# Performance work log

Measured on AMD Instinct MI355X. Metric: run time of the kernel, lower is better.

The kernel has to match this reference:

```python
import jax, jax.numpy as jnp
import numpy as np

EPS = 1e-8
VOX_WIDTH = 1.0
CURV_THRESH = 0.5


def _build_kernels():
    """Nine 3x3x3 central finite-difference stencils, pre-divided by vox_width / vox_width^2."""
    def zk():
        return np.zeros((3, 3, 3), np.float32)
    ks = {}
    # first derivatives (central difference), denominator vox_width
    for name, ax in (('ddx', 0), ('ddy', 1), ('ddz', 2)):
        k = zk(); i = [1, 1, 1]
        i[ax] = 0; k[tuple(i)] = -0.5
        i[ax] = 2; k[tuple(i)] = 0.5
        ks[name] = k / VOX_WIDTH
    # pure second derivatives, denominator vox_width^2
    for name, ax in (('d2dx2', 0), ('d2dy2', 1), ('d2dz2', 2)):
        k = zk(); i = [1, 1, 1]
        i[ax] = 0; k[tuple(i)] = 1.0
        i[ax] = 1; k[tuple(i)] = -2.0
        i[ax] = 2; k[tuple(i)] = 1.0
        ks[name] = k / VOX_WIDTH ** 2
    # mixed second derivatives, denominator vox_width^2
    for name, (a, b) in (('d2dxdy', (0, 1)), ('d2dxdz', (0, 2)), ('d2dydz', (1, 2))):
        k = zk()
        for sa, sb, v in ((0, 0, 0.25), (0, 2, -0.25), (2, 0, -0.25), (2, 2, 0.25)):
            i = [1, 1, 1]; i[a] = sa; i[b] = sb; k[tuple(i)] = v
        ks[name] = k / VOX_WIDTH ** 2
    order = ['ddx', 'ddy', 'ddz', 'd2dx2', 'd2dy2', 'd2dz2', 'd2dxdy', 'd2dxdz', 'd2dydz']
    return np.stack([ks[n] for n in order])[:, None]  # [9, 1, 3, 3, 3]


_KERNELS = jnp.asarray(_build_kernels())


def setup_inputs() -> dict:
    key = jax.random.key(0)
    phi = jax.random.normal(key, (2, 1, 192, 192, 192), dtype=jnp.float32)
    return {"phi": phi}


def reference(phi):
    # all nine stencils as one valid 3D conv: [N, 9, D-2, H-2, W-2]
    g = jax.lax.conv_general_dilated(
        phi, _KERNELS, window_strides=(1, 1, 1), padding='VALID',
        dimension_numbers=('NCDHW', 'OIDHW', 'NCDHW'))
    gx, gy, gz, hxx, hyy, hzz, hxy, hxz, hyz = (g[:, i:i + 1] for i in range(9))

    mag = jnp.sqrt(gx * gx + gy * gy + gz * gz + EPS)
    mag3 = mag ** 3

    # mean curvature: sum_{i!=j} g_i^2 H_jj - 2 sum_{i<j} g_i g_j H_ij, over |grad|^3
    cross = gx * gy * hxy + gx * gz * hxz + gy * gz * hyz
    mean_c = (gx * gx * (hyy + hzz) + gy * gy * (hxx + hzz) + gz * gz * (hxx + hyy)
              - 2.0 * cross) / (mag3 + EPS)

    # gaussian curvature: laplacian/|grad| - (g^T H g)/|grad|^3
    lap = (hxx + hyy + hzz) / (mag + EPS)
    quad = (gx * gx * hxx + gy * gy * hyy + gz * gz * hzz + 2.0 * cross) / (mag3 + EPS)
    gauss = lap - quad

    k1 = mean_c + jnp.sqrt(jnp.abs(mean_c ** 2 - gauss) + EPS)
    pen = jax.nn.relu((k1 / (CURV_THRESH + EPS)) ** 2 - 1.0)

    # zero crossings of phi over 3x3x3 neighborhoods (valid -> matches conv output shape)
    mn = jax.lax.reduce_window(phi, jnp.inf, jax.lax.min, (1, 1, 3, 3, 3), (1, 1, 1, 1, 1), 'VALID')
    mx = jax.lax.reduce_window(phi, -jnp.inf, jax.lax.max, (1, 1, 3, 3, 3), (1, 1, 1, 1, 1), 'VALID')
    phi_zero = jax.lax.stop_gradient((mn * mx < 0).astype(phi.dtype))

    return jnp.sum(phi_zero * pen) / (jnp.sum(phi_zero) + EPS)
```

## Files before the change

kernel.cpp:

```cpp
#include <hip/hip_runtime.h>


typedef float v2f __attribute__((ext_vector_type(2)));

constexpr int DIM  = 192;
constexpr int ODIM = 190;
constexpr int TX = 32, TY = 32, CZ = 10;
constexpr int NTX = 6, NTY = 6, NTZ = 19;
constexpr int PLANE = DIM * DIM;
constexpr int NBLOCKS = 2 * NTZ * NTY * NTX;

constexpr int LROW   = 40;
constexpr int LPLANE = 34 * LROW;

struct Slice {
    v2f   q[3][4];
    float xmn[4], xmx[4];
};

#define GLDS(srcp, dstp)                                                   \
    __builtin_amdgcn_global_load_lds(                                      \
        (const __attribute__((address_space(1))) void*)(srcp),             \
        (__attribute__((address_space(3))) void*)(dstp), 16, 0, 0)

#define WVM(n)  asm volatile("s_waitcnt vmcnt(" #n ")" ::: "memory")
#define BAR()   do { __builtin_amdgcn_s_barrier();                         \
                     asm volatile("" ::: "memory"); } while (0)

__global__ __launch_bounds__(256, 3) void curv_main(const float* __restrict__ phi,
                                                    double* __restrict__ acc,
                                                    int use_partials) {
    __shared__ float lds[4 * LPLANE];

    int bx = blockIdx.x;
    const int tx = bx % NTX; bx /= NTX;
    const int ty = bx % NTY; bx /= NTY;
    const int tz = bx % NTZ; bx /= NTZ;
    const int n  = bx;

    const int xbase = tx * TX, ybase = ty * TY, zbase = tz * CZ;
    const int tid = threadIdx.x;
    const int row = tid >> 3;
    const int x0  = (tid & 7) * 4;
    const float* pn  = phi + (long long)n * DIM * PLANE;
    const float* pzb = pn + (long long)zbase * PLANE;

    const int lane = tid & 63, wave = tid >> 6;
    const int chA = tid;
    const int chB = 256 + wave * 21 + lane;
    const bool bAct = lane < 21;
    int rA = ybase + chA / 10;       if (rA > DIM - 1) rA = DIM - 1;
    int cA = xbase + (chA % 10) * 4; if (cA > DIM - 4) cA = DIM - 4;
    const int offA = rA * DIM + cA;
    int rB = ybase + chB / 10;       if (rB > DIM - 1) rB = DIM - 1;
    int cB = xbase + (chB % 10) * 4; if (cB > DIM - 4) cB = DIM - 4;
    const int offB = rB * DIM + cB;

#define STAGE(g, bi) do {                                                  \
    const float* b_ = pzb + (g) * PLANE;                                   \
    GLDS(b_ + offA, &lds[(bi) * LPLANE + chA * 4]);                        \
    if (bAct) GLDS(b_ + offB, &lds[(bi) * LPLANE + chB * 4]);              \
} while (0)

    int lro[3];
#pragma unroll
    for (int dy = 0; dy < 3; ++dy) lro[dy] = (row + dy) * LROW;
    int c2r = x0 + 4;
    if (xbase + c2r > DIM - 2) c2r = DIM - 2 - xbase;

#define UNPACKL(S, bi) do {                                                \
    const float* lb_ = &lds[(bi) * LPLANE];                                \
    float mn6[6], mx6[6];                                                  \
    _Pragma("unroll")                                                      \
    for (int dy = 0; dy < 3; ++dy) {                                       \
        const float4 a = *(const float4*)(lb_ + lro[dy] + x0);             \
        const float2 b = *(const float2*)(lb_ + lro[dy] + c2r);            \
        (S).q[dy][0] = (v2f){a.x, a.z};                                    \
        (S).q[dy][1] = (v2f){a.y, a.w};                                    \
        (S).q[dy][2] = (v2f){a.z, b.x};                                    \
        (S).q[dy][3] = (v2f){a.w, b.y};                                    \
        if (dy == 0) {                                                     \
            mn6[0] = a.x; mn6[1] = a.y; mn6[2] = a.z;                      \
            mn6[3] = a.w; mn6[4] = b.x; mn6[5] = b.y;                      \
            mx6[0] = a.x; mx6[1] = a.y; mx6[2] = a.z;                      \
            mx6[3] = a.w; mx6[4] = b.x; mx6[5] = b.y;                      \
        } else {                                                           \
            mn6[0] = fminf(mn6[0], a.x); mx6[0] = fmaxf(mx6[0], a.x);      \
            mn6[1] = fminf(mn6[1], a.y); mx6[1] = fmaxf(mx6[1], a.y);      \
            mn6[2] = fminf(mn6[2], a.z); mx6[2] = fmaxf(mx6[2], a.z);      \
            mn6[3] = fminf(mn6[3], a.w); mx6[3] = fmaxf(mx6[3], a.w);      \
            mn6[4] = fminf(mn6[4], b.x); mx6[4] = fmaxf(mx6[4], b.x);      \
            mn6[5] = fminf(mn6[5], b.y); mx6[5] = fmaxf(mx6[5], b.y);      \
        }                                                                  \
    }                                                                      \
    _Pragma("unroll")                                                      \
    for (int j = 0; j < 4; ++j) {                                          \
        (S).xmn[j] = fminf(fminf(mn6[j], mn6[j + 1]), mn6[j + 2]);         \
        (S).xmx[j] = fmaxf(fmaxf(mx6[j], mx6[j + 1]), mx6[j + 2]);         \
    } } while (0)

    float fsp = 0.0f, fsc = 0.0f;
    const float EPSF = 1e-8f;
    const float EPS4 = 4e-8f;
    const int oy = ybase + row;

    bool vmask[4];
#pragma unroll
    for (int j = 0; j < 4; ++j)
        vmask[j] = (oy < ODIM) && (xbase + x0 + j < ODIM);

    auto compute = [&](const Slice& s0, const Slice& s1, const Slice& s2) {
        float wmn[4], wmx[4];
#pragma unroll
        for (int j = 0; j < 4; ++j) {
            wmn[j] = fminf(fminf(s0.xmn[j], s1.xmn[j]), s2.xmn[j]);
            wmx[j] = fmaxf(fmaxf(s0.xmx[j], s1.xmx[j]), s2.xmx[j]);
        }

#pragma unroll
        for (int p = 0; p < 2; ++p) {
            v2f Gx = s2.q[1][p + 1] - s0.q[1][p + 1];
            v2f Gy = s1.q[2][p + 1] - s1.q[0][p + 1];
            v2f Gz = s1.q[1][p + 2] - s1.q[1][p];

            v2f c2v = 2.0f * s1.q[1][p + 1];
            v2f hxx = s0.q[1][p + 1] - c2v + s2.q[1][p + 1];
            v2f hyy = s1.q[0][p + 1] - c2v + s1.q[2][p + 1];
            v2f hzz = s1.q[1][p] - c2v + s1.q[1][p + 2];

            v2f Mxy = s0.q[0][p + 1] - s0.q[2][p + 1]
                    - s2.q[0][p + 1] + s2.q[2][p + 1];
            v2f Mxz = s0.q[1][p] - s0.q[1][p + 2]
                    - s2.q[1][p] + s2.q[1][p + 2];
            v2f Myz = s1.q[0][p] - s1.q[0][p + 2]
                    - s1.q[2][p] + s1.q[2][p + 2];

            v2f Gx2 = Gx * Gx, Gy2 = Gy * Gy, Gz2 = Gz * Gz;
            v2f mag2G = Gx2 + Gy2 + Gz2 + EPS4;

            v2f r = (v2f){ __builtin_amdgcn_rsqf(mag2G.x),
                           __builtin_amdgcn_rsqf(mag2G.y) };
            v2f r3 = r * r * r;
            v2f twor3 = r3 + r3;

            v2f crossG = Gx * Gy * Mxy + Gx * Gz * Mxz + Gy * Gz * Myz;

            v2f num1 = Gx2 * (hyy + hzz) + Gy2 * (hxx + hzz) +
                       Gz2 * (hxx + hyy) - 0.5f * crossG;
            v2f mean_c = num1 * twor3;
            v2f lap   = (hxx + hyy + hzz) * (r + r);
            v2f num2  = Gx2 * hxx + Gy2 * hyy + Gz2 * hzz + 0.5f * crossG;
            v2f quad  = num2 * twor3;
            v2f gauss = lap - quad;

            v2f disc = mean_c * mean_c - gauss;
            v2f sq = (v2f){ sqrtf(fabsf(disc.x) + EPSF),
                            sqrtf(fabsf(disc.y) + EPSF) };
            v2f k1 = mean_c + sq;
            v2f t  = 2.0f * k1;
            v2f pen2 = t * t - 1.0f;

#pragma unroll
            for (int e = 0; e < 2; ++e) {
                const int j = p + 2 * e;
                float pen = fmaxf(e ? pen2.y : pen2.x, 0.0f);
                if (vmask[j] && (wmn[j] * wmx[j] < 0.0f)) {
                    fsp += pen;
                    fsc += 1.0f;
                }
            }
        }
    };

    Slice s0, s1, s2;

    STAGE(0, 0); STAGE(1, 1); STAGE(2, 2); STAGE(3, 3);
    WVM(6); BAR();
    UNPACKL(s0, 0);
    WVM(4); BAR();
    STAGE(4, 0);
    UNPACKL(s1, 1);
    WVM(4); BAR();
    STAGE(5, 1);

    UNPACKL(s2, 2); compute(s0, s1, s2); WVM(4); BAR(); STAGE(6, 2);
    UNPACKL(s0, 3); compute(s1, s2, s0); WVM(4); BAR(); STAGE(7, 3);
    UNPACKL(s1, 0); compute(s2, s0, s1); WVM(4); BAR(); STAGE(8, 0);
    UNPACKL(s2, 1); compute(s0, s1, s2); WVM(4); BAR(); STAGE(9, 1);
    UNPACKL(s0, 2); compute(s1, s2, s0); WVM(4); BAR(); STAGE(10, 2);
    UNPACKL(s1, 3); compute(s2, s0, s1); WVM(4); BAR(); STAGE(11, 3);
    UNPACKL(s2, 0); compute(s0, s1, s2); WVM(4); BAR();
    UNPACKL(s0, 1); compute(s1, s2, s0); WVM(2); BAR();
    UNPACKL(s1, 2); compute(s2, s0, s1); WVM(0); BAR();
    UNPACKL(s2, 3); compute(s0, s1, s2);

    double sp = (double)fsp, sc = (double)fsc;
#pragma unroll
    for (int off = 32; off > 0; off >>= 1) {
        sp += __shfl_down(sp, off, 64);
        sc += __shfl_down(sc, off, 64);
    }

    __shared__ double lsp[4], lsc[4];
    if (lane == 0) { lsp[wave] = sp; lsc[wave] = sc; }
    __syncthreads();
    if (tid == 0) {
        double tp = lsp[0] + lsp[1] + lsp[2] + lsp[3];
        double tc = lsc[0] + lsc[1] + lsc[2] + lsc[3];
        if (use_partials) {
            acc[2 * blockIdx.x]     = tp;
            acc[2 * blockIdx.x + 1] = tc;
        } else {
            atomicAdd(&acc[0], tp);
            atomicAdd(&acc[1], tc);
        }
    }
}

__global__ __launch_bounds__(256) void curv_reduce(const double* __restrict__ part,
                                                   int nblocks, int use_partials,
                                                   float* __restrict__ out) {
    double sp = 0.0, sc = 0.0;
    if (use_partials) {
        for (int i = threadIdx.x; i < nblocks; i += 256) {
            sp += part[2 * i];
            sc += part[2 * i + 1];
        }
    } else if (threadIdx.x == 0) {
        sp = part[0]; sc = part[1];
    }
#pragma unroll
    for (int off = 32; off > 0; off >>= 1) {
        sp += __shfl_down(sp, off, 64);
        sc += __shfl_down(sc, off, 64);
    }
    __shared__ double lsp[4], lsc[4];
    const int wave = threadIdx.x >> 6, lane = threadIdx.x & 63;
    if (lane == 0) { lsp[wave] = sp; lsc[wave] = sc; }
    __syncthreads();
    if (threadIdx.x == 0) {
        double tp = lsp[0] + lsp[1] + lsp[2] + lsp[3];
        double tc = lsc[0] + lsc[1] + lsc[2] + lsc[3];
        out[0] = (float)(tp / (tc + 1e-8));
    }
}

extern "C" void kernel_launch(void* const* d_in, const int* in_sizes, int n_in,
                              void* d_out, int out_size, void* d_ws, size_t ws_size,
                              hipStream_t stream) {
    const float* phi = (const float*)d_in[0];
    float* out = (float*)d_out;
    double* acc = (double*)d_ws;

    const int use_partials = (ws_size >= (size_t)(2 * NBLOCKS) * sizeof(double)) ? 1 : 0;
    if (!use_partials) {
        hipMemsetAsync(d_ws, 0, 2 * sizeof(double), stream);
    }

    curv_main<<<NBLOCKS, 256, 0, stream>>>(phi, acc, use_partials);
    curv_reduce<<<1, 256, 0, stream>>>(acc, NBLOCKS, use_partials, out);
}
```

Baseline: 111.6 us.

## Give each wave private LDS row windows and drop block barriers; deepen z-chunks

Each wave now stages its own 10-row halo window per plane into a private LDS region, so the per-plane block-wide barriers become per-wave waitcnt (vmcnt plus lgkmcnt). The z-chunk per block grows from 10 to 19 planes, halving the number of z tiles and the halo re-reads along z. The costs are duplicated halo rows between neighbouring waves (10 rows loaded per 8 used), a larger LDS footprint that may limit occupancy, and fewer blocks for load balancing.

```diff
diff --git a/kernel.cpp b/kernel.cpp
--- a/kernel.cpp
+++ b/kernel.cpp
@@ -5,13 +5,14 @@
 
 constexpr int DIM  = 192;
 constexpr int ODIM = 190;
-constexpr int TX = 32, TY = 32, CZ = 10;
-constexpr int NTX = 6, NTY = 6, NTZ = 19;
+constexpr int TX = 32, TY = 32, CZ = 19;
+constexpr int NTX = 6, NTY = 6, NTZ = 10;
 constexpr int PLANE = DIM * DIM;
 constexpr int NBLOCKS = 2 * NTZ * NTY * NTX;
 
-constexpr int LROW   = 40;
-constexpr int LPLANE = 34 * LROW;
+constexpr int WROWS = 10;
+constexpr int LROW  = 40;
+constexpr int WPL   = WROWS * LROW;
 
 struct Slice {
     v2f   q[3][4];
@@ -23,14 +24,12 @@
         (const __attribute__((address_space(1))) void*)(srcp),             \
         (__attribute__((address_space(3))) void*)(dstp), 16, 0, 0)
 
-#define WVM(n)  asm volatile("s_waitcnt vmcnt(" #n ")" ::: "memory")
-#define BAR()   do { __builtin_amdgcn_s_barrier();                         \
-                     asm volatile("" ::: "memory"); } while (0)
+#define WVMLG(n) asm volatile("s_waitcnt vmcnt(" #n ") lgkmcnt(0)" ::: "memory")
 
 __global__ __launch_bounds__(256, 3) void curv_main(const float* __restrict__ phi,
                                                     double* __restrict__ acc,
                                                     int use_partials) {
-    __shared__ float lds[4 * LPLANE];
+    __shared__ float lds[4 * 4 * WPL];
 
     int bx = blockIdx.x;
     const int tx = bx % NTX; bx /= NTX;
@@ -40,36 +39,37 @@
 
     const int xbase = tx * TX, ybase = ty * TY, zbase = tz * CZ;
     const int tid = threadIdx.x;
+    const int lane = tid & 63, wave = tid >> 6;
     const int row = tid >> 3;
-    const int x0  = (tid & 7) * 4;
+    const int x0  = (lane & 7) * 4;
     const float* pn  = phi + (long long)n * DIM * PLANE;
     const float* pzb = pn + (long long)zbase * PLANE;
 
-    const int lane = tid & 63, wave = tid >> 6;
-    const int chA = tid;
-    const int chB = 256 + wave * 21 + lane;
-    const bool bAct = lane < 21;
-    int rA = ybase + chA / 10;       if (rA > DIM - 1) rA = DIM - 1;
-    int cA = xbase + (chA % 10) * 4; if (cA > DIM - 4) cA = DIM - 4;
+    const int chA = lane;
+    const int chB = 64 + lane;
+    const bool bAct = lane < 36;
+    int rA = ybase + wave * 8 + chA / 10; if (rA > DIM - 1) rA = DIM - 1;
+    int cA = xbase + (chA % 10) * 4;      if (cA > DIM - 4) cA = DIM - 4;
     const int offA = rA * DIM + cA;
-    int rB = ybase + chB / 10;       if (rB > DIM - 1) rB = DIM - 1;
-    int cB = xbase + (chB % 10) * 4; if (cB > DIM - 4) cB = DIM - 4;
+    int rB = ybase + wave * 8 + chB / 10; if (rB > DIM - 1) rB = DIM - 1;
+    int cB = xbase + (chB % 10) * 4;      if (cB > DIM - 4) cB = DIM - 4;
     const int offB = rB * DIM + cB;
 
 #define STAGE(g, bi) do {                                                  \
     const float* b_ = pzb + (g) * PLANE;                                   \
-    GLDS(b_ + offA, &lds[(bi) * LPLANE + chA * 4]);                        \
-    if (bAct) GLDS(b_ + offB, &lds[(bi) * LPLANE + chB * 4]);              \
+    float* w_ = &lds[((bi) * 4 + wave) * WPL];                             \
+    GLDS(b_ + offA, w_ + chA * 4);                                         \
+    if (bAct) GLDS(b_ + offB, w_ + chB * 4);                               \
 } while (0)
 
     int lro[3];
 #pragma unroll
-    for (int dy = 0; dy < 3; ++dy) lro[dy] = (row + dy) * LROW;
+    for (int dy = 0; dy < 3; ++dy) lro[dy] = ((lane >> 3) + dy) * LROW;
     int c2r = x0 + 4;
     if (xbase + c2r > DIM - 2) c2r = DIM - 2 - xbase;
 
 #define UNPACKL(S, bi) do {                                                \
-    const float* lb_ = &lds[(bi) * LPLANE];                                \
+    const float* lb_ = &lds[((bi) * 4 + wave) * WPL];                      \
     float mn6[6], mx6[6];                                                  \
     _Pragma("unroll")                                                      \
     for (int dy = 0; dy < 3; ++dy) {                                       \
@@ -175,24 +175,33 @@
     Slice s0, s1, s2;
 
     STAGE(0, 0); STAGE(1, 1); STAGE(2, 2); STAGE(3, 3);
-    WVM(6); BAR();
+    WVMLG(6);
     UNPACKL(s0, 0);
-    WVM(4); BAR();
+    WVMLG(4);
     STAGE(4, 0);
     UNPACKL(s1, 1);
-    WVM(4); BAR();
+    WVMLG(4);
     STAGE(5, 1);
 
-    UNPACKL(s2, 2); compute(s0, s1, s2); WVM(4); BAR(); STAGE(6, 2);
-    UNPACKL(s0, 3); compute(s1, s2, s0); WVM(4); BAR(); STAGE(7, 3);
-    UNPACKL(s1, 0); compute(s2, s0, s1); WVM(4); BAR(); STAGE(8, 0);
-    UNPACKL(s2, 1); compute(s0, s1, s2); WVM(4); BAR(); STAGE(9, 1);
-    UNPACKL(s0, 2); compute(s1, s2, s0); WVM(4); BAR(); STAGE(10, 2);
-    UNPACKL(s1, 3); compute(s2, s0, s1); WVM(4); BAR(); STAGE(11, 3);
-    UNPACKL(s2, 0); compute(s0, s1, s2); WVM(4); BAR();
-    UNPACKL(s0, 1); compute(s1, s2, s0); WVM(2); BAR();
-    UNPACKL(s1, 2); compute(s2, s0, s1); WVM(0); BAR();
-    UNPACKL(s2, 3); compute(s0, s1, s2);
+    UNPACKL(s2, 2); compute(s0, s1, s2); WVMLG(4); STAGE(6, 2);
+    UNPACKL(s0, 3); compute(s1, s2, s0); WVMLG(4); STAGE(7, 3);
+    UNPACKL(s1, 0); compute(s2, s0, s1); WVMLG(4); STAGE(8, 0);
+    UNPACKL(s2, 1); compute(s0, s1, s2); WVMLG(4); STAGE(9, 1);
+    UNPACKL(s0, 2); compute(s1, s2, s0); WVMLG(4); STAGE(10, 2);
+    UNPACKL(s1, 3); compute(s2, s0, s1); WVMLG(4); STAGE(11, 3);
+    UNPACKL(s2, 0); compute(s0, s1, s2); WVMLG(4); STAGE(12, 0);
+    UNPACKL(s0, 1); compute(s1, s2, s0); WVMLG(4); STAGE(13, 1);
+    UNPACKL(s1, 2); compute(s2, s0, s1); WVMLG(4); STAGE(14, 2);
+    UNPACKL(s2, 3); compute(s0, s1, s2); WVMLG(4); STAGE(15, 3);
+    UNPACKL(s0, 0); compute(s1, s2, s0); WVMLG(4); STAGE(16, 0);
+    UNPACKL(s1, 1); compute(s2, s0, s1); WVMLG(4); STAGE(17, 1);
+    UNPACKL(s2, 2); compute(s0, s1, s2); WVMLG(4); STAGE(18, 2);
+    UNPACKL(s0, 3); compute(s1, s2, s0); WVMLG(4); STAGE(19, 3);
+    UNPACKL(s1, 0); compute(s2, s0, s1); WVMLG(4); STAGE(20, 0);
+    UNPACKL(s2, 1); compute(s0, s1, s2); WVMLG(4);
+    UNPACKL(s0, 2); compute(s1, s2, s0); WVMLG(2);
+    UNPACKL(s1, 3); compute(s2, s0, s1); WVMLG(0);
+    UNPACKL(s2, 0); compute(s0, s1, s2);
 
     double sp = (double)fsp, sc = (double)fsc;
 #pragma unroll
```

New measurement: 109.3 us. 2.1% less time.
